# Kernel tuning notes

Hardware: AMD Instinct MI355X
Metric: run time of the kernel (lower is better)

## Reference

```python
import jax, jax.numpy as jnp
import numpy as np

B, T, H, V = 256, 256, 512, 32000
L = 3  # stacked LSTM layers


def setup_inputs() -> dict:
    key = jax.random.key(0)
    ks = jax.random.split(key, 12)
    s = 0.05
    n = lambda k, shp: (jax.random.normal(k, shp, jnp.float32) * s)
    return {
        "text_1": jax.random.randint(ks[0], (B, T), 0, V, dtype=jnp.int32),
        "text_2": jax.random.randint(ks[1], (B, T), 0, V, dtype=jnp.int32),
        "text_3": jax.random.randint(ks[2], (B, T), 0, V, dtype=jnp.int32),
        "emb": n(ks[3], (V, H)),
        "Wx": n(ks[4], (L, H, 4 * H)),
        "Wh": n(ks[5], (L, H, 4 * H)),
        "b": jnp.zeros((L, 4 * H), jnp.float32),
        "g1": jnp.ones((3 * H,), jnp.float32), "beta1": jnp.zeros((3 * H,), jnp.float32),
        "W1": n(ks[6], (3 * H, 2 * H)), "bd1": jnp.zeros((2 * H,), jnp.float32),
        "g2": jnp.ones((2 * H,), jnp.float32), "beta2": jnp.zeros((2 * H,), jnp.float32),
        "W2": n(ks[7], (2 * H, H // 5)), "bd2": jnp.zeros((H // 5,), jnp.float32),
        "g3": jnp.ones((H // 5,), jnp.float32), "beta3": jnp.zeros((H // 5,), jnp.float32),
        "W3": n(ks[8], (H // 5, 4)), "bd3": jnp.zeros((4,), jnp.float32),
    }


def _lstm_stack(tokens, emb, Wx, Wh, b):
    # tokens: [B, T] int -> last hidden of top layer [B, H]
    x = emb[tokens]                      # [B, T, H]
    x = jnp.transpose(x, (1, 0, 2))      # [T, B, H] (scan over time)
    bsz, h = x.shape[1], Wh.shape[1]
    for l in range(Wx.shape[0]):
        Wx_l, Wh_l, b_l = Wx[l], Wh[l], b[l]
        def step(carry, xt):
            hprev, cprev = carry
            gates = xt @ Wx_l + hprev @ Wh_l + b_l      # [B, 4H]
            i, f, g, o = jnp.split(gates, 4, axis=-1)
            c = jax.nn.sigmoid(f) * cprev + jax.nn.sigmoid(i) * jnp.tanh(g)
            hnew = jax.nn.sigmoid(o) * jnp.tanh(c)
            return (hnew, c), hnew
        init = (jnp.zeros((bsz, h), x.dtype), jnp.zeros((bsz, h), x.dtype))
        _, x = jax.lax.scan(step, init, x)
    return x[-1]                          # rnn_output[:, -1, :]


def _bn(x, gamma, beta, eps=1e-3):
    m = jnp.mean(x, axis=0)
    v = jnp.var(x, axis=0)
    return gamma * (x - m) * jax.lax.rsqrt(v + eps) + beta


def reference(text_1, text_2, text_3, emb, Wx, Wh, b,
              g1, beta1, W1, bd1, g2, beta2, W2, bd2, g3, beta3, W3, bd3):
    r1 = _lstm_stack(text_1, emb, Wx, Wh, b)
    r2 = _lstm_stack(text_2, emb, Wx, Wh, b)
    r3 = _lstm_stack(text_3, emb, Wx, Wh, b)
    r = jnp.concatenate([r1, r2, r3], axis=1)   # [B, 3H]
    r = _bn(r, g1, beta1)
    r = jax.nn.selu(r @ W1 + bd1)
    r = _bn(r, g2, beta2)
    r = jax.nn.selu(r @ W2 + bd2)
    r = _bn(r, g3, beta3)
    return r @ W3 + bd3                          # [B, 4] logits
```

## Files before the change

kernel.cpp:

```cpp
#include <hip/hip_runtime.h>
#include <hip/hip_bf16.h>

typedef __attribute__((ext_vector_type(8))) short short8;
typedef __attribute__((ext_vector_type(4))) float floatx4;

namespace {
constexpr int kB1 = 256;
constexpr int kT  = 256;
constexpr int kH  = 512;
constexpr int kL  = 3;
constexpr int kB3 = 768;
constexpr int kK  = 1024;
constexpr int kN  = 2048;
constexpr size_t kHB = (size_t)kB3 * kH;

constexpr size_t WREP_OFF   = 0;
constexpr size_t WREP_BYTES = (size_t)kL * kK * kN * 2;
constexpr size_t BREP_OFF   = WREP_OFF + WREP_BYTES;
constexpr size_t BREP_BYTES = (size_t)kL * kN * 4;
constexpr size_t HBUF_OFF   = BREP_OFF + BREP_BYTES;
constexpr size_t HBUF_BYTES = (size_t)kL * 2 * kHB * 2;
constexpr size_t CBUF_OFF   = HBUF_OFF + HBUF_BYTES;
constexpr size_t CBUF_BYTES = (size_t)kL * kHB * 4;
constexpr size_t BNA_OFF    = CBUF_OFF + CBUF_BYTES;
constexpr size_t BNC_OFF    = BNA_OFF + 1536 * 4;
constexpr size_t Z1_OFF     = BNC_OFF + 1536 * 4;
constexpr size_t Z2_OFF     = Z1_OFF + (size_t)256 * 1024 * 4;
constexpr size_t FLAG_OFF   = Z2_OFF + (size_t)256 * 102 * 4;
constexpr size_t BAR_OFF    = FLAG_OFF + 128;
constexpr int kPersistGrid  = 768;
}

__device__ __forceinline__ float ldf(const void* p, size_t idx, int isf32) {
  if (isf32) return ((const float*)p)[idx];
  return __bfloat162float(((const __hip_bfloat16*)p)[idx]);
}

__device__ __forceinline__ short f2bs(float x) {
  union { __hip_bfloat16 h; short s; } u;
  u.h = __float2bfloat16(x);
  return u.s;
}

__device__ __forceinline__ short8 cvt8(const float* q) {
  float4 lo = *(const float4*)q;
  float4 hi = *(const float4*)(q + 4);
  short8 v;
  v[0] = f2bs(lo.x); v[1] = f2bs(lo.y); v[2] = f2bs(lo.z); v[3] = f2bs(lo.w);
  v[4] = f2bs(hi.x); v[5] = f2bs(hi.y); v[6] = f2bs(hi.z); v[7] = f2bs(hi.w);
  return v;
}

__device__ __forceinline__ short8 ldg16_coh(const void* p) {
  short8 v;
  asm volatile("global_load_dwordx4 %0, %1, off sc0 sc1"
               : "=v"(v) : "v"(p) : "memory");
  return v;
}

__global__ void detect_kernel(const unsigned* __restrict__ g1, int* __restrict__ flag,
                              unsigned* __restrict__ bar) {
  int tid = threadIdx.x;
  if (tid < 256)
    __hip_atomic_store(&bar[tid], 0u, __ATOMIC_RELAXED, __HIP_MEMORY_SCOPE_AGENT);
  if (tid == 0 && blockIdx.x == 0)
    *flag = (g1[0] == 0x3F800000u) ? 1 : 0;
}

__global__ __launch_bounds__(256) void repack_kernel(
    const void* __restrict__ Wx, const void* __restrict__ Wh,
    const void* __restrict__ bias, const int* __restrict__ flagp,
    __hip_bfloat16* __restrict__ Wrep, float* __restrict__ brep) {
  int isf32 = *flagp;
  int idx = blockIdx.x * 256 + threadIdx.x;
  if (idx >= kL * kK * kN) return;
  int j  = idx & 7;
  int n2 = (idx >> 3) & (kN - 1);
  int kg = (idx >> 14) & 127;
  int l  = idx >> 21;
  int k  = kg * 8 + j;
  int ntile = n2 >> 7, c = n2 & 127, g = c >> 5, ul = c & 31;
  int u = ntile * 32 + ul;
  int col = g * 512 + u;
  float v;
  if (k < kH) v = ldf(Wx, ((size_t)l * kH + k) * kN + col, isf32);
  else        v = ldf(Wh, ((size_t)l * kH + (k - kH)) * kN + col, isf32);
  Wrep[idx] = __float2bfloat16(v);
  if (kg == 0 && j == 0) brep[l * kN + n2] = ldf(bias, (size_t)l * kN + col, isf32);
}

__device__ __forceinline__ void grid_barrier(unsigned* bar, int bid, int tid) {
  __syncthreads();
  if (tid == 0) {
    unsigned* cnt  = bar + (bid & 7) * 16;
    unsigned* gcnt = bar + 128;
    unsigned* gen  = bar + 160;
    __threadfence();
    unsigned g = __hip_atomic_load(gen, __ATOMIC_RELAXED, __HIP_MEMORY_SCOPE_AGENT);
    unsigned a = __hip_atomic_fetch_add(cnt, 1u, __ATOMIC_ACQ_REL, __HIP_MEMORY_SCOPE_AGENT);
    if (a == (kPersistGrid / 8) - 1u) {
      __hip_atomic_store(cnt, 0u, __ATOMIC_RELAXED, __HIP_MEMORY_SCOPE_AGENT);
      unsigned ga = __hip_atomic_fetch_add(gcnt, 1u, __ATOMIC_ACQ_REL, __HIP_MEMORY_SCOPE_AGENT);
      if (ga == 7u) {
        __hip_atomic_store(gcnt, 0u, __ATOMIC_RELAXED, __HIP_MEMORY_SCOPE_AGENT);
        __hip_atomic_store(gen, g + 1u, __ATOMIC_RELEASE, __HIP_MEMORY_SCOPE_AGENT);
      }
    }
    long long t0 = (long long)__builtin_amdgcn_s_memrealtime();
    while (__hip_atomic_load(gen, __ATOMIC_ACQUIRE, __HIP_MEMORY_SCOPE_AGENT) == g) {
      __builtin_amdgcn_s_sleep(2);
      if ((long long)__builtin_amdgcn_s_memrealtime() - t0 > 20000000LL) break;
    }
  }
  __syncthreads();
}

__global__ __launch_bounds__(256, 3) void persist_kernel(
    const __hip_bfloat16* __restrict__ Wrep, const float* __restrict__ brep,
    __hip_bfloat16* __restrict__ hbuf, const void* __restrict__ emb,
    const int* __restrict__ flagp, const int* __restrict__ t1,
    const int* __restrict__ t2, const int* __restrict__ t3,
    unsigned* __restrict__ bar) {
  __shared__ __align__(16) char smem[26624];

  const int tid = threadIdx.x;
  const int bid = blockIdx.x;
  const int l   = bid >> 8;
  const int mt  = (bid >> 4) & 15;
  const int nt  = bid & 15;
  const int wv = tid >> 6, lane = tid & 63, lm = lane & 15, lq = lane >> 4;
  const int isf32 = *flagp;
  const int r0   = tid >> 4;
  const int kcol = (tid & 15) * 8;

  const int R0 = mt * 48 + r0, R1 = R0 + 16, R2 = R0 + 32;
  const int* tb0 = nullptr; const int* tb1 = nullptr; const int* tb2 = nullptr;
  if (l == 0) {
    tb0 = (((R0 >> 8) == 0) ? t1 : ((R0 >> 8) == 1) ? t2 : t3) + (R0 & 255) * kT;
    tb1 = (((R1 >> 8) == 0) ? t1 : ((R1 >> 8) == 1) ? t2 : t3) + (R1 & 255) * kT;
    tb2 = (((R2 >> 8) == 0) ? t1 : ((R2 >> 8) == 1) ? t2 : t3) + (R2 & 255) * kT;
  }
  const unsigned ro0 = (unsigned)R0 * kH + kcol;
  const unsigned ro1 = (unsigned)R1 * kH + kcol;
  const unsigned ro2 = (unsigned)R2 * kH + kcol;

  const __hip_bfloat16* WB = Wrep + (size_t)l * kK * kN;
  const int n0w = nt * 128 + wv * 32;
  const float bv0 = brep[l * kN + n0w + lm];
  const float bv1 = brep[l * kN + n0w + 16 + lm];

  char* aw0 = smem + r0 * 272 + (tid & 15) * 16;
  char* aw1 = aw0 + 16 * 272;
  char* aw2 = aw0 + 32 * 272;
  const char* ar = smem + lm * 272 + lq * 16;

  const int cuu = tid & 31, crow = tid >> 5;
  float creg[6] = {0.f, 0.f, 0.f, 0.f, 0.f, 0.f};

#pragma unroll 1
  for (int s = 0; s < kT + kL - 1; s++) {
    const int t = s - l;
    if (t >= 0 && t < kT) {
      const __hip_bfloat16* hp = hbuf + ((size_t)l * 2 + ((t & 1) ^ 1)) * kHB;
      const __hip_bfloat16* xh = nullptr;
      const void *xe0 = nullptr, *xe1 = nullptr, *xe2 = nullptr;
      if (l == 0) {
        int k0 = tb0[t], k1 = tb1[t], k2 = tb2[t];
        if (isf32) {
          xe0 = (const void*)((const float*)emb + (size_t)k0 * kH + kcol);
          xe1 = (const void*)((const float*)emb + (size_t)k1 * kH + kcol);
          xe2 = (const void*)((const float*)emb + (size_t)k2 * kH + kcol);
        } else {
          xe0 = (const void*)((const __hip_bfloat16*)emb + (size_t)k0 * kH + kcol);
          xe1 = (const void*)((const __hip_bfloat16*)emb + (size_t)k1 * kH + kcol);
          xe2 = (const void*)((const __hip_bfloat16*)emb + (size_t)k2 * kH + kcol);
        }
      } else {
        xh = hbuf + ((size_t)(l - 1) * 2 + (t & 1)) * kHB;
      }

      auto loadA = [&](int sl, short8& d0, short8& d1, short8& d2) {
        if (sl < 4) {
          if (l == 0) {
            if (isf32) {
              d0 = cvt8((const float*)xe0 + sl * 128);
              d1 = cvt8((const float*)xe1 + sl * 128);
              d2 = cvt8((const float*)xe2 + sl * 128);
            } else {
              d0 = *(const short8*)((const __hip_bfloat16*)xe0 + sl * 128);
              d1 = *(const short8*)((const __hip_bfloat16*)xe1 + sl * 128);
              d2 = *(const short8*)((const __hip_bfloat16*)xe2 + sl * 128);
            }
          } else {
            d0 = ldg16_coh(xh + ro0 + sl * 128);
            d1 = ldg16_coh(xh + ro1 + sl * 128);
            d2 = ldg16_coh(xh + ro2 + sl * 128);
          }
        } else if (t == 0) {
          short8 z = {0, 0, 0, 0, 0, 0, 0, 0};
          d0 = z; d1 = z; d2 = z;
        } else {
          d0 = ldg16_coh(hp + ro0 + (sl - 4) * 128);
          d1 = ldg16_coh(hp + ro1 + (sl - 4) * 128);
          d2 = ldg16_coh(hp + ro2 + (sl - 4) * 128);
        }
      };

      floatx4 zf = {0.f, 0.f, 0.f, 0.f};
      floatx4 acc[3][2];
#pragma unroll
      for (int a = 0; a < 3; a++) { acc[a][0] = zf; acc[a][1] = zf; }

      short8 avA0, avA1, avA2, avB0, avB1, avB2;
      loadA(0, avA0, avA1, avA2);

#pragma unroll
      for (int sl = 0; sl < 8; sl++) {
        __syncthreads();
        asm volatile("s_waitcnt vmcnt(0)" ::: "memory");
        if ((sl & 1) == 0) {
          *(short8*)aw0 = avA0; *(short8*)aw1 = avA1; *(short8*)aw2 = avA2;
          if (sl < 7) loadA(sl + 1, avB0, avB1, avB2);
        } else {
          *(short8*)aw0 = avB0; *(short8*)aw1 = avB1; *(short8*)aw2 = avB2;
          if (sl < 7) loadA(sl + 1, avA0, avA1, avA2);
        }
        short8 bfrag[4][2];
#pragma unroll
        for (int kk = 0; kk < 4; kk++)
#pragma unroll
          for (int nf = 0; nf < 2; nf++) {
            int kg = sl * 16 + kk * 4 + lq;
            bfrag[kk][nf] = *(const short8*)(WB + ((size_t)kg * kN + n0w + nf * 16 + lm) * 8);
          }
        __syncthreads();
#pragma unroll
        for (int kk = 0; kk < 4; kk++) {
          short8 af0 = *(const short8*)(ar + 0 * 4352 + kk * 64);
          short8 af1 = *(const short8*)(ar + 1 * 4352 + kk * 64);
          short8 af2 = *(const short8*)(ar + 2 * 4352 + kk * 64);
          acc[0][0] = __builtin_amdgcn_mfma_f32_16x16x32_bf16(af0, bfrag[kk][0], acc[0][0], 0, 0, 0);
          acc[0][1] = __builtin_amdgcn_mfma_f32_16x16x32_bf16(af0, bfrag[kk][1], acc[0][1], 0, 0, 0);
          acc[1][0] = __builtin_amdgcn_mfma_f32_16x16x32_bf16(af1, bfrag[kk][0], acc[1][0], 0, 0, 0);
          acc[1][1] = __builtin_amdgcn_mfma_f32_16x16x32_bf16(af1, bfrag[kk][1], acc[1][1], 0, 0, 0);
          acc[2][0] = __builtin_amdgcn_mfma_f32_16x16x32_bf16(af2, bfrag[kk][0], acc[2][0], 0, 0, 0);
          acc[2][1] = __builtin_amdgcn_mfma_f32_16x16x32_bf16(af2, bfrag[kk][1], acc[2][1], 0, 0, 0);
        }
      }

      __syncthreads();
      float* gl = (float*)smem;
#pragma unroll
      for (int mf = 0; mf < 3; mf++)
#pragma unroll
        for (int nf = 0; nf < 2; nf++)
#pragma unroll
          for (int r = 0; r < 4; r++) {
            int rowf = mf * 16 + lq * 4 + r;
            gl[(wv * 48 + rowf) * 34 + nf * 16 + lm] = acc[mf][nf][r] + (nf ? bv1 : bv0);
          }
      __syncthreads();

      __hip_bfloat16* hout = hbuf + ((size_t)l * 2 + (t & 1)) * kHB;
#pragma unroll
      for (int ii = 0; ii < 6; ii++) {
        int rowf = crow + 8 * ii;
        float gi = fminf(fmaxf(gl[(0 * 48 + rowf) * 34 + cuu], -40.f), 40.f);
        float gf = fminf(fmaxf(gl[(1 * 48 + rowf) * 34 + cuu], -40.f), 40.f);
        float gg = fminf(fmaxf(gl[(2 * 48 + rowf) * 34 + cuu], -40.f), 40.f);
        float go = fminf(fmaxf(gl[(3 * 48 + rowf) * 34 + cuu], -40.f), 40.f);
        float c_old = (t > 0) ? creg[ii] : 0.f;
        float si = 1.f / (1.f + __expf(-gi));
        float sf = 1.f / (1.f + __expf(-gf));
        float so = 1.f / (1.f + __expf(-go));
        float cn = sf * c_old + si * tanhf(gg);
        float hn = so * tanhf(cn);
        creg[ii] = cn;
        union { __hip_bfloat16 h; unsigned short u; } cv;
        cv.h = __float2bfloat16(hn);
        __hip_atomic_store(
            (unsigned short*)(hout + (size_t)(mt * 48 + rowf) * kH + nt * 32 + cuu),
            cv.u, __ATOMIC_RELAXED, __HIP_MEMORY_SCOPE_AGENT);
      }
    }
    if (s < kT + kL - 2) grid_barrier(bar, bid, tid);
  }
}

__global__ __launch_bounds__(256) void step_kernel(
    int s,
    const __hip_bfloat16* __restrict__ Wrep, const float* __restrict__ brep,
    __hip_bfloat16* __restrict__ hbuf, float* __restrict__ cbuf,
    const void* __restrict__ emb, const int* __restrict__ flagp,
    const int* __restrict__ t1, const int* __restrict__ t2, const int* __restrict__ t3) {
  __shared__ __align__(16) char smem[34816];

  int bid = blockIdx.x;
  int l  = bid / 192;
  int rr = bid % 192;
  int nt = rr & 15;
  int mt = rr >> 4;
  int t = s - l;
  if (t < 0 || t >= kT) return;

  int isf32 = *flagp;
  int tid = threadIdx.x;
  int wv = tid >> 6, lane = tid & 63;
  int lm = lane & 15, lq = lane >> 4;

  int arow = tid >> 2;
  int kc   = tid & 3;
  int row_g = mt * 64 + arow;

  const void* xsrc;
  bool xf32 = false;
  if (l == 0) {
    int i = row_g >> 8, bb = row_g & 255;
    const int* txt = (i == 0) ? t1 : (i == 1) ? t2 : t3;
    int tok = txt[bb * kT + t];
    if (isf32) { xsrc = (const void*)((const float*)emb + (size_t)tok * kH); xf32 = true; }
    else         xsrc = (const void*)((const __hip_bfloat16*)emb + (size_t)tok * kH);
  } else {
    const __hip_bfloat16* hIn = hbuf + ((size_t)(l - 1) * 2 + (t & 1)) * kHB;
    xsrc = (const void*)(hIn + (size_t)row_g * kH);
  }
  const __hip_bfloat16* hrow = nullptr;
  if (t > 0) {
    const __hip_bfloat16* hPrev = hbuf + ((size_t)l * 2 + ((t & 1) ^ 1)) * kHB;
    hrow = hPrev + (size_t)row_g * kH;
  }

  floatx4 zf = {0.f, 0.f, 0.f, 0.f};
  floatx4 acc[4][2];
#pragma unroll
  for (int a = 0; a < 4; a++)
#pragma unroll
    for (int b = 0; b < 2; b++) acc[a][b] = zf;

  const __hip_bfloat16* WB = Wrep + (size_t)l * kK * kN;
  int n0w = nt * 128 + wv * 32;

#pragma unroll 1
  for (int sl = 0; sl < 8; sl++) {
    short8 bfrag[4][2];
#pragma unroll
    for (int kk = 0; kk < 4; kk++)
#pragma unroll
      for (int nf = 0; nf < 2; nf++) {
        size_t kg = (size_t)(sl * 16 + kk * 4 + lq);
        const __hip_bfloat16* p = WB + (kg * kN + (n0w + nf * 16 + lm)) * 8;
        bfrag[kk][nf] = *(const short8*)p;
      }
    short8 av[4];
    bool zero = (sl >= 4) && (t == 0);
    if (!zero) {
      if (sl < 4 && xf32) {
        const float* sf = (const float*)xsrc + sl * 128;
#pragma unroll
        for (int jj = 0; jj < 4; jj++) {
          const float* q = sf + kc * 8 + jj * 32;
          float4 lo = *(const float4*)q;
          float4 hi = *(const float4*)(q + 4);
          short8 v;
          v[0] = f2bs(lo.x); v[1] = f2bs(lo.y); v[2] = f2bs(lo.z); v[3] = f2bs(lo.w);
          v[4] = f2bs(hi.x); v[5] = f2bs(hi.y); v[6] = f2bs(hi.z); v[7] = f2bs(hi.w);
          av[jj] = v;
        }
      } else {
        const __hip_bfloat16* src = (sl < 4)
            ? ((const __hip_bfloat16*)xsrc + sl * 128)
            : (hrow + (sl - 4) * 128);
#pragma unroll
        for (int jj = 0; jj < 4; jj++)
          av[jj] = *(const short8*)(src + kc * 8 + jj * 32);
      }
    } else {
      short8 vz = {0, 0, 0, 0, 0, 0, 0, 0};
#pragma unroll
      for (int jj = 0; jj < 4; jj++) av[jj] = vz;
    }
    __syncthreads();
#pragma unroll
    for (int jj = 0; jj < 4; jj++) {
      int klocal = kc * 8 + jj * 32;
      *(short8*)(smem + arow * 272 + klocal * 2) = av[jj];
    }
    __syncthreads();
#pragma unroll
    for (int kk = 0; kk < 4; kk++) {
      short8 afrag[4];
#pragma unroll
      for (int mf = 0; mf < 4; mf++) {
        int rowf = mf * 16 + lm;
        afrag[mf] = *(const short8*)(smem + rowf * 272 + kk * 64 + lq * 16);
      }
#pragma unroll
      for (int mf = 0; mf < 4; mf++)
#pragma unroll
        for (int nf = 0; nf < 2; nf++)
          acc[mf][nf] = __builtin_amdgcn_mfma_f32_16x16x32_bf16(
              afrag[mf], bfrag[kk][nf], acc[mf][nf], 0, 0, 0);
    }
  }

  const float* bl = brep + l * kN;
#pragma unroll
  for (int nf = 0; nf < 2; nf++) {
    float bv = bl[n0w + nf * 16 + lm];
#pragma unroll
    for (int mf = 0; mf < 4; mf++)
#pragma unroll
      for (int r = 0; r < 4; r++) acc[mf][nf][r] += bv;
  }

  __syncthreads();
  float* gl = (float*)smem;
#pragma unroll
  for (int mf = 0; mf < 4; mf++)
#pragma unroll
    for (int nf = 0; nf < 2; nf++)
#pragma unroll
      for (int r = 0; r < 4; r++) {
        int rowf = mf * 16 + lq * 4 + r;
        int uu   = nf * 16 + lm;
        gl[((size_t)wv * 64 + rowf) * 34 + uu] = acc[mf][nf][r];
      }
  __syncthreads();

  float* cl = cbuf + (size_t)l * kHB;
  __hip_bfloat16* hout = hbuf + ((size_t)l * 2 + (t & 1)) * kHB;
#pragma unroll
  for (int ii = 0; ii < 8; ii++) {
    int idx = tid + 256 * ii;
    int uu = idx & 31, rowf = idx >> 5;
    float gi = fminf(fmaxf(gl[(0 * 64 + rowf) * 34 + uu], -40.f), 40.f);
    float gf = fminf(fmaxf(gl[(1 * 64 + rowf) * 34 + uu], -40.f), 40.f);
    float gg = fminf(fmaxf(gl[(2 * 64 + rowf) * 34 + uu], -40.f), 40.f);
    float go = fminf(fmaxf(gl[(3 * 64 + rowf) * 34 + uu], -40.f), 40.f);
    int bg = mt * 64 + rowf;
    int ug = nt * 32 + uu;
    size_t off = (size_t)bg * kH + ug;
    float c_old = (t > 0) ? cl[off] : 0.f;
    float si = 1.f / (1.f + __expf(-gi));
    float sf = 1.f / (1.f + __expf(-gf));
    float so = 1.f / (1.f + __expf(-go));
    float cn = sf * c_old + si * tanhf(gg);
    float hn = so * tanhf(cn);
    cl[off] = cn;
    hout[off] = __float2bfloat16(hn);
  }
}

__global__ __launch_bounds__(256) void stats_kernel(
    int ncols, int mode, const void* __restrict__ src,
    const void* __restrict__ gamma, const void* __restrict__ beta,
    const int* __restrict__ flagp, float* __restrict__ bn_a, float* __restrict__ bn_c) {
  int isf32 = *flagp;
  int col = blockIdx.x * 256 + threadIdx.x;
  if (col >= ncols) return;
  float sum = 0.f, ss = 0.f;
  for (int b = 0; b < kB1; b++) {
    float v;
    if (mode == 0) {
      const __hip_bfloat16* h = (const __hip_bfloat16*)src;
      v = __bfloat162float(h[((size_t)((col >> 9) * kB1 + b)) * kH + (col & 511)]);
    } else {
      v = ((const float*)src)[(size_t)b * ncols + col];
    }
    v = fmaxf(-1e15f, fminf(v, 1e15f));
    sum += v; ss += v * v;
  }
  float mean = sum * (1.f / kB1);
  float var  = ss * (1.f / kB1) - mean * mean;
  float a = ldf(gamma, col, isf32) * rsqrtf(var + 1e-3f);
  bn_a[col] = a;
  bn_c[col] = ldf(beta, col, isf32) - mean * a;
}

__global__ __launch_bounds__(256) void headgemm_kernel(
    int Kd, int Nd, int mode, const void* __restrict__ Asrc,
    const float* __restrict__ bn_a, const float* __restrict__ bn_c,
    const void* __restrict__ W, const void* __restrict__ bias,
    const int* __restrict__ flagp, float* __restrict__ out, int do_selu) {
  __shared__ float As[32][65];
  __shared__ float Bs[32][65];
  int isf32 = *flagp;
  int tid = threadIdx.x;
  int bx = blockIdx.x, by = blockIdx.y;
  int tx = tid & 15, ty = tid >> 4;
  float acc[4][4] = {};
  int am = tid & 63, ak = tid >> 6;
  int bk = tid >> 3, bn8 = (tid & 7) * 8;
  for (int ks = 0; ks < Kd; ks += 32) {
    __syncthreads();
    for (int jj = 0; jj < 8; jj++) {
      int kl = ak * 8 + jj;
      int kg = ks + kl;
      int mg = by * 64 + am;
      float v;
      if (mode == 0) {
        const __hip_bfloat16* h = (const __hip_bfloat16*)Asrc;
        v = __bfloat162float(h[((size_t)((kg >> 9) * kB1 + mg)) * kH + (kg & 511)]);
      } else {
        v = ((const float*)Asrc)[(size_t)mg * Kd + kg];
      }
      As[kl][am] = v * bn_a[kg] + bn_c[kg];
    }
    for (int e = 0; e < 8; e++) {
      int col = bx * 64 + bn8 + e;
      Bs[bk][bn8 + e] = (col < Nd) ? ldf(W, (size_t)(ks + bk) * Nd + col, isf32) : 0.f;
    }
    __syncthreads();
    for (int k = 0; k < 32; k++) {
      float ar[4], br[4];
#pragma unroll
      for (int i = 0; i < 4; i++) ar[i] = As[k][ty * 4 + i];
#pragma unroll
      for (int j = 0; j < 4; j++) br[j] = Bs[k][tx * 4 + j];
#pragma unroll
      for (int i = 0; i < 4; i++)
#pragma unroll
        for (int j = 0; j < 4; j++) acc[i][j] += ar[i] * br[j];
    }
  }
  for (int i = 0; i < 4; i++) {
    int row = by * 64 + ty * 4 + i;
    for (int j = 0; j < 4; j++) {
      int col = bx * 64 + tx * 4 + j;
      if (col < Nd) {
        float y = acc[i][j] + ldf(bias, col, isf32);
        if (do_selu)
          y = (y > 0.f) ? 1.0507009873554805f * y
                        : 1.0507009873554805f * 1.6732632423543772f * (__expf(y) - 1.f);
        out[(size_t)row * Nd + col] = y;
      }
    }
  }
}

__global__ __launch_bounds__(256) void final_kernel(
    const float* __restrict__ z2, const float* __restrict__ bn_a, const float* __restrict__ bn_c,
    const void* __restrict__ W3, const void* __restrict__ bd3,
    const int* __restrict__ flagp, void* __restrict__ out) {
  int isf32 = *flagp;
  int b = threadIdx.x;
  float acc[4] = {0.f, 0.f, 0.f, 0.f};
  for (int j = 0; j < 102; j++) {
    float y = z2[b * 102 + j] * bn_a[j] + bn_c[j];
#pragma unroll
    for (int g = 0; g < 4; g++) acc[g] += y * ldf(W3, j * 4 + g, isf32);
  }
#pragma unroll
  for (int g = 0; g < 4; g++) {
    float y = acc[g] + ldf(bd3, g, isf32);
    if (isf32) ((float*)out)[b * 4 + g] = y;
    else ((__hip_bfloat16*)out)[b * 4 + g] = __float2bfloat16(y);
  }
}

extern "C" void kernel_launch(void* const* d_in, const int* in_sizes, int n_in,
                              void* d_out, int out_size, void* d_ws, size_t ws_size,
                              hipStream_t stream) {
  const int* t1 = (const int*)d_in[0];
  const int* t2 = (const int*)d_in[1];
  const int* t3 = (const int*)d_in[2];
  const void* emb = d_in[3];
  const void* Wx  = d_in[4];
  const void* Wh  = d_in[5];
  const void* bb  = d_in[6];
  const void* g1  = d_in[7];
  const void* be1 = d_in[8];
  const void* W1  = d_in[9];
  const void* bd1 = d_in[10];
  const void* g2  = d_in[11];
  const void* be2 = d_in[12];
  const void* W2  = d_in[13];
  const void* bd2 = d_in[14];
  const void* g3  = d_in[15];
  const void* be3 = d_in[16];
  const void* W3  = d_in[17];
  const void* bd3 = d_in[18];

  char* ws = (char*)d_ws;
  __hip_bfloat16* Wrep = (__hip_bfloat16*)(ws + WREP_OFF);
  float* brep = (float*)(ws + BREP_OFF);
  __hip_bfloat16* hbuf = (__hip_bfloat16*)(ws + HBUF_OFF);
  float* cbuf = (float*)(ws + CBUF_OFF);
  float* bn_a = (float*)(ws + BNA_OFF);
  float* bn_c = (float*)(ws + BNC_OFF);
  float* z1 = (float*)(ws + Z1_OFF);
  float* z2 = (float*)(ws + Z2_OFF);
  int* flag = (int*)(ws + FLAG_OFF);
  unsigned* bar = (unsigned*)(ws + BAR_OFF);

  static int persist_ok = -1;
  if (persist_ok < 0) {
    int nb = 0, ncu = 0, dev = 0;
    (void)hipGetDevice(&dev);
    (void)hipDeviceGetAttribute(&ncu, hipDeviceAttributeMultiprocessorCount, dev);
    hipError_t e = hipOccupancyMaxActiveBlocksPerMultiprocessor(&nb, persist_kernel, 256, 0);
    persist_ok = (e == hipSuccess && (long)nb * (long)ncu >= kPersistGrid) ? 1 : 0;
  }

  detect_kernel<<<1, 256, 0, stream>>>((const unsigned*)g1, flag, bar);

  repack_kernel<<<(kL * kK * kN) / 256, 256, 0, stream>>>(Wx, Wh, bb, flag, Wrep, brep);

  if (persist_ok) {
    persist_kernel<<<kPersistGrid, 256, 0, stream>>>(
        Wrep, brep, hbuf, emb, flag, t1, t2, t3, bar);
  } else {
    for (int s = 0; s < kT + kL - 1; s++)
      step_kernel<<<3 * 192, 256, 0, stream>>>(s, Wrep, brep, hbuf, cbuf, emb, flag, t1, t2, t3);
  }

  const __hip_bfloat16* hTop = hbuf + (2 * 2 + 1) * kHB;
  stats_kernel<<<6, 256, 0, stream>>>(1536, 0, hTop, g1, be1, flag, bn_a, bn_c);
  headgemm_kernel<<<dim3(16, 4), 256, 0, stream>>>(1536, 1024, 0, hTop, bn_a, bn_c, W1, bd1, flag, z1, 1);
  stats_kernel<<<4, 256, 0, stream>>>(1024, 1, z1, g2, be2, flag, bn_a, bn_c);
  headgemm_kernel<<<dim3(2, 4), 256, 0, stream>>>(1024, 102, 1, z1, bn_a, bn_c, W2, bd2, flag, z2, 1);
  stats_kernel<<<1, 256, 0, stream>>>(102, 1, z2, g3, be3, flag, bn_a, bn_c);
  final_kernel<<<1, 256, 0, stream>>>(z2, bn_a, bn_c, W3, bd3, flag, (void*)d_out);
}
```

Before: 6.054 ms.

## Prefetch next-step weights and embeddings across barrier, swizzle LDS, relax barrier fences

Restructures the persistent LSTM step loop. Weight fragments are now double-buffered alongside activations, the first weight slice and the layer-0 embedding rows for the next timestep are prefetched before the grid barrier, and token indices are read one step ahead. The LDS A tile uses an XOR swizzle instead of padding to avoid bank conflicts. The grid barrier drops the threadfence and acquire spin in favour of a single acquire fence after the barrier, and the hidden-state loads become plain loads instead of sc0/sc1 coherent loads. Plain loads of hbuf written by other blocks may return stale cached data, and the extra double-buffered registers may cost occupancy.

```diff
diff --git a/kernel.cpp b/kernel.cpp
--- a/kernel.cpp
+++ b/kernel.cpp
@@ -48,13 +48,6 @@
   short8 v;
   v[0] = f2bs(lo.x); v[1] = f2bs(lo.y); v[2] = f2bs(lo.z); v[3] = f2bs(lo.w);
   v[4] = f2bs(hi.x); v[5] = f2bs(hi.y); v[6] = f2bs(hi.z); v[7] = f2bs(hi.w);
-  return v;
-}
-
-__device__ __forceinline__ short8 ldg16_coh(const void* p) {
-  short8 v;
-  asm volatile("global_load_dwordx4 %0, %1, off sc0 sc1"
-               : "=v"(v) : "v"(p) : "memory");
   return v;
 }
 
@@ -95,7 +88,6 @@
     unsigned* cnt  = bar + (bid & 7) * 16;
     unsigned* gcnt = bar + 128;
     unsigned* gen  = bar + 160;
-    __threadfence();
     unsigned g = __hip_atomic_load(gen, __ATOMIC_RELAXED, __HIP_MEMORY_SCOPE_AGENT);
     unsigned a = __hip_atomic_fetch_add(cnt, 1u, __ATOMIC_ACQ_REL, __HIP_MEMORY_SCOPE_AGENT);
     if (a == (kPersistGrid / 8) - 1u) {
@@ -107,12 +99,13 @@
       }
     }
     long long t0 = (long long)__builtin_amdgcn_s_memrealtime();
-    while (__hip_atomic_load(gen, __ATOMIC_ACQUIRE, __HIP_MEMORY_SCOPE_AGENT) == g) {
+    while (__hip_atomic_load(gen, __ATOMIC_RELAXED, __HIP_MEMORY_SCOPE_AGENT) == g) {
       __builtin_amdgcn_s_sleep(2);
       if ((long long)__builtin_amdgcn_s_memrealtime() - t0 > 20000000LL) break;
     }
   }
   __syncthreads();
+  __builtin_amdgcn_fence(__ATOMIC_ACQUIRE, "agent");
 }
 
 __global__ __launch_bounds__(256, 3) void persist_kernel(
@@ -131,14 +124,17 @@
   const int wv = tid >> 6, lane = tid & 63, lm = lane & 15, lq = lane >> 4;
   const int isf32 = *flagp;
   const int r0   = tid >> 4;
-  const int kcol = (tid & 15) * 8;
+  const int c16  = tid & 15;
+  const int kcol = c16 * 8;
 
   const int R0 = mt * 48 + r0, R1 = R0 + 16, R2 = R0 + 32;
   const int* tb0 = nullptr; const int* tb1 = nullptr; const int* tb2 = nullptr;
+  int tk0 = 0, tk1 = 0, tk2 = 0;
   if (l == 0) {
     tb0 = (((R0 >> 8) == 0) ? t1 : ((R0 >> 8) == 1) ? t2 : t3) + (R0 & 255) * kT;
     tb1 = (((R1 >> 8) == 0) ? t1 : ((R1 >> 8) == 1) ? t2 : t3) + (R1 & 255) * kT;
     tb2 = (((R2 >> 8) == 0) ? t1 : ((R2 >> 8) == 1) ? t2 : t3) + (R2 & 255) * kT;
+    tk0 = tb0[0]; tk1 = tb1[0]; tk2 = tb2[0];
   }
   const unsigned ro0 = (unsigned)R0 * kH + kcol;
   const unsigned ro1 = (unsigned)R1 * kH + kcol;
@@ -149,13 +145,19 @@
   const float bv0 = brep[l * kN + n0w + lm];
   const float bv1 = brep[l * kN + n0w + 16 + lm];
 
-  char* aw0 = smem + r0 * 272 + (tid & 15) * 16;
-  char* aw1 = aw0 + 16 * 272;
-  char* aw2 = aw0 + 32 * 272;
-  const char* ar = smem + lm * 272 + lq * 16;
+  char* aw0 = smem + r0 * 256 + ((c16 ^ (r0 & 7)) << 4);
+  char* aw1 = aw0 + 16 * 256;
+  char* aw2 = aw0 + 32 * 256;
+  const char* arb = smem + lm * 256;
+  int oswz[4];
+#pragma unroll
+  for (int kk = 0; kk < 4; kk++) oswz[kk] = (((kk * 4 + lq) ^ (lm & 7)) << 4);
 
   const int cuu = tid & 31, crow = tid >> 5;
   float creg[6] = {0.f, 0.f, 0.f, 0.f, 0.f, 0.f};
+
+  short8 aA0, aA1, aA2, aB0, aB1, aB2;
+  short8 bA[4][2], bB[4][2];
 
 #pragma unroll 1
   for (int s = 0; s < kT + kL - 1; s++) {
@@ -164,17 +166,18 @@
       const __hip_bfloat16* hp = hbuf + ((size_t)l * 2 + ((t & 1) ^ 1)) * kHB;
       const __hip_bfloat16* xh = nullptr;
       const void *xe0 = nullptr, *xe1 = nullptr, *xe2 = nullptr;
+      int nk0 = 0, nk1 = 0, nk2 = 0;
       if (l == 0) {
-        int k0 = tb0[t], k1 = tb1[t], k2 = tb2[t];
         if (isf32) {
-          xe0 = (const void*)((const float*)emb + (size_t)k0 * kH + kcol);
-          xe1 = (const void*)((const float*)emb + (size_t)k1 * kH + kcol);
-          xe2 = (const void*)((const float*)emb + (size_t)k2 * kH + kcol);
+          xe0 = (const void*)((const float*)emb + (size_t)tk0 * kH + kcol);
+          xe1 = (const void*)((const float*)emb + (size_t)tk1 * kH + kcol);
+          xe2 = (const void*)((const float*)emb + (size_t)tk2 * kH + kcol);
         } else {
-          xe0 = (const void*)((const __hip_bfloat16*)emb + (size_t)k0 * kH + kcol);
-          xe1 = (const void*)((const __hip_bfloat16*)emb + (size_t)k1 * kH + kcol);
-          xe2 = (const void*)((const __hip_bfloat16*)emb + (size_t)k2 * kH + kcol);
+          xe0 = (const void*)((const __hip_bfloat16*)emb + (size_t)tk0 * kH + kcol);
+          xe1 = (const void*)((const __hip_bfloat16*)emb + (size_t)tk1 * kH + kcol);
+          xe2 = (const void*)((const __hip_bfloat16*)emb + (size_t)tk2 * kH + kcol);
         }
+        if (t + 1 < kT) { nk0 = tb0[t + 1]; nk1 = tb1[t + 1]; nk2 = tb2[t + 1]; }
       } else {
         xh = hbuf + ((size_t)(l - 1) * 2 + (t & 1)) * kHB;
       }
@@ -192,59 +195,59 @@
               d2 = *(const short8*)((const __hip_bfloat16*)xe2 + sl * 128);
             }
           } else {
-            d0 = ldg16_coh(xh + ro0 + sl * 128);
-            d1 = ldg16_coh(xh + ro1 + sl * 128);
-            d2 = ldg16_coh(xh + ro2 + sl * 128);
+            d0 = *(const short8*)(xh + ro0 + sl * 128);
+            d1 = *(const short8*)(xh + ro1 + sl * 128);
+            d2 = *(const short8*)(xh + ro2 + sl * 128);
           }
         } else if (t == 0) {
           short8 z = {0, 0, 0, 0, 0, 0, 0, 0};
           d0 = z; d1 = z; d2 = z;
         } else {
-          d0 = ldg16_coh(hp + ro0 + (sl - 4) * 128);
-          d1 = ldg16_coh(hp + ro1 + (sl - 4) * 128);
-          d2 = ldg16_coh(hp + ro2 + (sl - 4) * 128);
+          d0 = *(const short8*)(hp + ro0 + (sl - 4) * 128);
+          d1 = *(const short8*)(hp + ro1 + (sl - 4) * 128);
+          d2 = *(const short8*)(hp + ro2 + (sl - 4) * 128);
         }
       };
+      auto loadB = [&](int sl, short8 (&bf)[4][2]) {
+#pragma unroll
+        for (int kk = 0; kk < 4; kk++)
+#pragma unroll
+          for (int nf = 0; nf < 2; nf++) {
+            int kg = sl * 16 + kk * 4 + lq;
+            bf[kk][nf] = *(const short8*)(WB + ((size_t)kg * kN + n0w + nf * 16 + lm) * 8);
+          }
+      };
+
+      if (l != 0 || t == 0) loadA(0, aA0, aA1, aA2);
+      if (t == 0) loadB(0, bA);
 
       floatx4 zf = {0.f, 0.f, 0.f, 0.f};
       floatx4 acc[3][2];
 #pragma unroll
       for (int a = 0; a < 3; a++) { acc[a][0] = zf; acc[a][1] = zf; }
 
-      short8 avA0, avA1, avA2, avB0, avB1, avB2;
-      loadA(0, avA0, avA1, avA2);
-
 #pragma unroll
       for (int sl = 0; sl < 8; sl++) {
         __syncthreads();
-        asm volatile("s_waitcnt vmcnt(0)" ::: "memory");
-        if ((sl & 1) == 0) {
-          *(short8*)aw0 = avA0; *(short8*)aw1 = avA1; *(short8*)aw2 = avA2;
-          if (sl < 7) loadA(sl + 1, avB0, avB1, avB2);
-        } else {
-          *(short8*)aw0 = avB0; *(short8*)aw1 = avB1; *(short8*)aw2 = avB2;
-          if (sl < 7) loadA(sl + 1, avA0, avA1, avA2);
+        if ((sl & 1) == 0) { *(short8*)aw0 = aA0; *(short8*)aw1 = aA1; *(short8*)aw2 = aA2; }
+        else               { *(short8*)aw0 = aB0; *(short8*)aw1 = aB1; *(short8*)aw2 = aB2; }
+        __syncthreads();
+        if (sl < 7) {
+          if ((sl & 1) == 0) { loadA(sl + 1, aB0, aB1, aB2); loadB(sl + 1, bB); }
+          else               { loadA(sl + 1, aA0, aA1, aA2); loadB(sl + 1, bA); }
         }
-        short8 bfrag[4][2];
-#pragma unroll
-        for (int kk = 0; kk < 4; kk++)
-#pragma unroll
-          for (int nf = 0; nf < 2; nf++) {
-            int kg = sl * 16 + kk * 4 + lq;
-            bfrag[kk][nf] = *(const short8*)(WB + ((size_t)kg * kN + n0w + nf * 16 + lm) * 8);
-          }
-        __syncthreads();
 #pragma unroll
         for (int kk = 0; kk < 4; kk++) {
-          short8 af0 = *(const short8*)(ar + 0 * 4352 + kk * 64);
-          short8 af1 = *(const short8*)(ar + 1 * 4352 + kk * 64);
-          short8 af2 = *(const short8*)(ar + 2 * 4352 + kk * 64);
-          acc[0][0] = __builtin_amdgcn_mfma_f32_16x16x32_bf16(af0, bfrag[kk][0], acc[0][0], 0, 0, 0);
-          acc[0][1] = __builtin_amdgcn_mfma_f32_16x16x32_bf16(af0, bfrag[kk][1], acc[0][1], 0, 0, 0);
-          acc[1][0] = __builtin_amdgcn_mfma_f32_16x16x32_bf16(af1, bfrag[kk][0], acc[1][0], 0, 0, 0);
-          acc[1][1] = __builtin_amdgcn_mfma_f32_16x16x32_bf16(af1, bfrag[kk][1], acc[1][1], 0, 0, 0);
-          acc[2][0] = __builtin_amdgcn_mfma_f32_16x16x32_bf16(af2, bfrag[kk][0], acc[2][0], 0, 0, 0);
-          acc[2][1] = __builtin_amdgcn_mfma_f32_16x16x32_bf16(af2, bfrag[kk][1], acc[2][1], 0, 0, 0);
+          const short8* bf = (sl & 1) ? &bB[kk][0] : &bA[kk][0];
+          short8 af0 = *(const short8*)(arb + 0 * 4096 + oswz[kk]);
+          short8 af1 = *(const short8*)(arb + 1 * 4096 + oswz[kk]);
+          short8 af2 = *(const short8*)(arb + 2 * 4096 + oswz[kk]);
+          acc[0][0] = __builtin_amdgcn_mfma_f32_16x16x32_bf16(af0, bf[0], acc[0][0], 0, 0, 0);
+          acc[0][1] = __builtin_amdgcn_mfma_f32_16x16x32_bf16(af0, bf[1], acc[0][1], 0, 0, 0);
+          acc[1][0] = __builtin_amdgcn_mfma_f32_16x16x32_bf16(af1, bf[0], acc[1][0], 0, 0, 0);
+          acc[1][1] = __builtin_amdgcn_mfma_f32_16x16x32_bf16(af1, bf[1], acc[1][1], 0, 0, 0);
+          acc[2][0] = __builtin_amdgcn_mfma_f32_16x16x32_bf16(af2, bf[0], acc[2][0], 0, 0, 0);
+          acc[2][1] = __builtin_amdgcn_mfma_f32_16x16x32_bf16(af2, bf[1], acc[2][1], 0, 0, 0);
         }
       }
 
@@ -281,6 +284,23 @@
         __hip_atomic_store(
             (unsigned short*)(hout + (size_t)(mt * 48 + rowf) * kH + nt * 32 + cuu),
             cv.u, __ATOMIC_RELAXED, __HIP_MEMORY_SCOPE_AGENT);
+      }
+
+      if (t + 1 < kT) {
+        loadB(0, bA);
+        if (l == 0) {
+          tk0 = nk0; tk1 = nk1; tk2 = nk2;
+          if (isf32) {
+            xe0 = (const void*)((const float*)emb + (size_t)tk0 * kH + kcol);
+            xe1 = (const void*)((const float*)emb + (size_t)tk1 * kH + kcol);
+            xe2 = (const void*)((const float*)emb + (size_t)tk2 * kH + kcol);
+          } else {
+            xe0 = (const void*)((const __hip_bfloat16*)emb + (size_t)tk0 * kH + kcol);
+            xe1 = (const void*)((const __hip_bfloat16*)emb + (size_t)tk1 * kH + kcol);
+            xe2 = (const void*)((const __hip_bfloat16*)emb + (size_t)tk2 * kH + kcol);
+          }
+          loadA(0, aA0, aA1, aA2);
+        }
       }
     }
     if (s < kT + kL - 2) grid_barrier(bar, bid, tid);
```

New measurement: 6.011 ms. About the same (-0.7%).
